# Kernel tuning notes

Hardware: AMD Instinct MI355X
Metric: run time of the kernel (lower is better)

Reference implementation:

```python
import jax, jax.numpy as jnp
import numpy as np

SEQ, BATCH, D_IN, D_HID, D_OUT = 2048, 256, 512, 512, 1000


def setup_inputs() -> dict:
    key = jax.random.key(0)
    ks = jax.random.split(key, 15)
    s_in = 1.0 / np.sqrt(D_IN)
    s_h = 1.0 / np.sqrt(D_HID)
    def lin(k, fan_in, shape, scale):
        return jax.random.uniform(k, shape, jnp.float32, -scale, scale)
    return {
        "x": jax.random.normal(ks[0], (SEQ, BATCH, D_IN), jnp.float32),
        # weights stored as [in, out] so y = x @ W + b
        "Wz": lin(ks[1], D_IN, (D_IN, D_HID), s_in),  "bz": lin(ks[2], D_IN, (D_HID,), s_in),
        "Uz": lin(ks[3], D_HID, (D_HID, D_HID), s_h), "buz": lin(ks[4], D_HID, (D_HID,), s_h),
        "Wr": lin(ks[5], D_IN, (D_IN, D_HID), s_in),  "br": lin(ks[6], D_IN, (D_HID,), s_in),
        "Ur": lin(ks[7], D_HID, (D_HID, D_HID), s_h), "bur": lin(ks[8], D_HID, (D_HID,), s_h),
        "Wh": lin(ks[9], D_IN, (D_IN, D_HID), s_in),  "bh": lin(ks[10], D_IN, (D_HID,), s_in),
        "Uh": lin(ks[11], D_HID, (D_HID, D_HID), s_h), "buh": lin(ks[12], D_HID, (D_HID,), s_h),
        "Wfc": lin(ks[13], D_HID, (D_HID, D_OUT), s_h), "bfc": lin(ks[14], D_HID, (D_OUT,), s_h),
    }


def reference(x, Wz, bz, Uz, buz, Wr, br, Ur, bur, Wh, bh, Uh, buh, Wfc, bfc):
    B, H = x.shape[1], Uz.shape[0]

    def gru_step(h, xt):
        # xt: [B, D_IN], h: [B, H]
        z = jax.nn.sigmoid(xt @ Wz + bz + h @ Uz + buz)
        r = jax.nn.sigmoid(xt @ Wr + br + h @ Ur + bur)
        h_tild = jnp.tanh(xt @ Wh + bh + (r * h) @ Uh + buh)
        h_new = (1.0 - z) * h + z * h_tild
        return h_new, None

    h0 = jnp.zeros((B, H), x.dtype)  # zero init hidden (broadcast-equivalent)
    h, _ = jax.lax.scan(gru_step, h0, x)
    out = jax.nn.relu(h) @ Wfc + bfc        # [B, D_OUT]
    out = out[None]                          # [1, B, D_OUT]
    return jax.nn.log_softmax(out, axis=1)  # dim=1 as in torch module
```

## Files before the change

kernel.cpp:

```cpp
#include <hip/hip_runtime.h>


typedef unsigned short ushort_t;
typedef unsigned int uint_t;
typedef __bf16 bf16_t;
typedef bf16_t bf16x8 __attribute__((ext_vector_type(8)));
typedef float f32x4 __attribute__((ext_vector_type(4)));
typedef uint_t u32x4 __attribute__((ext_vector_type(4)));

__device__ __forceinline__ ushort_t f2bf(float f) {
  uint_t u = __float_as_uint(f);
  u += 0x7FFFu + ((u >> 16) & 1u);
  return (ushort_t)(u >> 16);
}
__device__ __forceinline__ float bf2f(ushort_t h) {
  return __uint_as_float(((uint_t)h) << 16);
}

__device__ __forceinline__ uint_t atom_add_ret(uint_t* p, uint_t v) {
  uint_t old;
  asm volatile("global_atomic_add %0, %1, %2, off sc0\n\t"
               "s_waitcnt vmcnt(0)"
               : "=v"(old) : "v"(p), "v"(v) : "memory");
  return old;
}

__global__ __launch_bounds__(256) void prep_kernel(
    const float* __restrict__ Wz, const float* __restrict__ Wr, const float* __restrict__ Wh,
    const float* __restrict__ Uz, const float* __restrict__ Ur, const float* __restrict__ Uh,
    const float* __restrict__ bz, const float* __restrict__ buz,
    const float* __restrict__ br, const float* __restrict__ bur,
    const float* __restrict__ bh, const float* __restrict__ buh,
    ushort_t* __restrict__ UT, ushort_t* __restrict__ WT, float* __restrict__ gbias)
{
  const int idx = blockIdx.x * 256 + threadIdx.x;
  {
    const int gate = idx >> 18, n = (idx >> 9) & 511, k = idx & 511;
    const float* U = (gate == 0) ? Uz : (gate == 1 ? Ur : Uh);
    UT[idx] = f2bf(U[k * 512 + n]);
  }
  {
    const int n = idx >> 9, k = idx & 511;
    const int gate = n >> 9, nn = n & 511;
    const float* W = (gate == 0) ? Wz : (gate == 1 ? Wr : Wh);
    WT[idx] = f2bf(W[k * 512 + nn]);
  }
  if (idx < 1536) {
    const int gate = idx >> 9, nn = idx & 511;
    gbias[idx] = (gate == 0) ? (bz[nn] + buz[nn])
               : (gate == 1) ? (br[nn] + bur[nn])
                             : (bh[nn] + buh[nn]);
  }
}

__global__ __launch_bounds__(256) void gate_gemm(
    const float* __restrict__ x,
    const ushort_t* __restrict__ WT,
    const float* __restrict__ gbias,
    ushort_t* __restrict__ gout,
    int mtiles)
{
  __shared__ ushort_t A_sh[128 * 72];
  __shared__ ushort_t B_sh[128 * 72];
  const int bid = blockIdx.x;
  int mt, nt;
  if ((mtiles & 31) == 0) {
    const int sb = bid / 384;
    const int r = bid - sb * 384;
    mt = sb * 32 + (r & 31);
    nt = r >> 5;
  } else {
    mt = bid / 12;
    nt = bid - mt * 12;
  }
  const int mrow0 = mt * 128;
  const int ncol0 = nt * 128;
  const int tid = threadIdx.x;
  const int wid = tid >> 6;
  const int lane = tid & 63;
  const int wm = wid >> 1, wn = wid & 1;
  const int l15 = lane & 15, l4 = lane >> 4;

  const f32x4 vzero = {0.f, 0.f, 0.f, 0.f};
  f32x4 acc[4][4];
#pragma unroll
  for (int m = 0; m < 4; ++m) {
#pragma unroll
    for (int n = 0; n < 4; ++n) acc[m][n] = vzero;
  }

  const int ar = tid >> 4;
  const int ak = tid & 15;
  const int bn = tid >> 3;
  const int bk = tid & 7;

  for (int ks = 0; ks < 8; ++ks) {
    if (ks) __syncthreads();
    const int k0 = ks * 64;
#pragma unroll
    for (int p = 0; p < 8; ++p) {
      const int r = p * 16 + ar;
      const float4 v = *(const float4*)&x[(size_t)(mrow0 + r) * 512 + (k0 + ak * 4)];
      ushort4 hv;
      hv.x = f2bf(v.x); hv.y = f2bf(v.y); hv.z = f2bf(v.z); hv.w = f2bf(v.w);
      *(ushort4*)&A_sh[r * 72 + ak * 4] = hv;
    }
#pragma unroll
    for (int p = 0; p < 4; ++p) {
      const int n = p * 32 + bn;
      *(uint4*)&B_sh[n * 72 + bk * 8] =
          *(const uint4*)&WT[(size_t)(ncol0 + n) * 512 + (k0 + bk * 8)];
    }
    __syncthreads();
#pragma unroll
    for (int kk = 0; kk < 2; ++kk) {
      bf16x8 a[4], b[4];
#pragma unroll
      for (int m = 0; m < 4; ++m)
        a[m] = *(const bf16x8*)&A_sh[(wm * 64 + m * 16 + l15) * 72 + kk * 32 + l4 * 8];
#pragma unroll
      for (int n = 0; n < 4; ++n)
        b[n] = *(const bf16x8*)&B_sh[(wn * 64 + n * 16 + l15) * 72 + kk * 32 + l4 * 8];
#pragma unroll
      for (int m = 0; m < 4; ++m) {
#pragma unroll
        for (int n = 0; n < 4; ++n)
          acc[m][n] = __builtin_amdgcn_mfma_f32_16x16x32_bf16(a[m], b[n], acc[m][n], 0, 0, 0);
      }
    }
  }
#pragma unroll
  for (int n = 0; n < 4; ++n) {
    const int gcol = ncol0 + wn * 64 + n * 16 + l15;
    const float bv = gbias[gcol];
#pragma unroll
    for (int m = 0; m < 4; ++m) {
      const int grow = mrow0 + wm * 64 + m * 16 + l4 * 4;
#pragma unroll
      for (int q = 0; q < 4; ++q)
        gout[(size_t)(grow + q) * 1536 + gcol] = f2bf(acc[m][n][q] + bv);
    }
  }
}

__device__ __forceinline__ bool group_barrier(uint_t* ctr, uint_t target, int tid, int* s_dead) {
  asm volatile("s_waitcnt vmcnt(0)" ::: "memory");
  __syncthreads();
  if (tid == 0) {
    uint_t seen = atom_add_ret(ctr, 1u) + 1u;
    int cnt = 0;
    while (seen < target) {
      __builtin_amdgcn_s_sleep(1);
      seen = atom_add_ret(ctr, 0u);
      if (++cnt > (1 << 15)) { *s_dead = 1; break; }
    }
  }
  __syncthreads();
  return *s_dead != 0;
}

__device__ __forceinline__ void stage16x512(const ushort_t* __restrict__ src, int g,
                                            ushort_t* dst_lds, int tid) {
  const ushort_t* p[4];
#pragma unroll
  for (int k = 0; k < 4; ++k) {
    const int idx = tid + (k << 8);
    const int r = idx >> 6, kc = idx & 63;
    p[k] = src + (((g * 16 + r) << 9) + kc * 8);
  }
  u32x4 v0, v1, v2, v3;
  asm volatile(
      "global_load_dwordx4 %0, %4, off sc0\n\t"
      "global_load_dwordx4 %1, %5, off sc0\n\t"
      "global_load_dwordx4 %2, %6, off sc0\n\t"
      "global_load_dwordx4 %3, %7, off sc0\n\t"
      "s_waitcnt vmcnt(0)"
      : "=&v"(v0), "=&v"(v1), "=&v"(v2), "=&v"(v3)
      : "v"(p[0]), "v"(p[1]), "v"(p[2]), "v"(p[3])
      : "memory");
#pragma unroll
  for (int k = 0; k < 4; ++k) {
    const int idx = tid + (k << 8);
    const int r = idx >> 6, kc = idx & 63;
    *(u32x4*)&dst_lds[r * 520 + kc * 8] = (k == 0) ? v0 : (k == 1) ? v1 : (k == 2) ? v2 : v3;
  }
}

__global__ __launch_bounds__(256, 1) void gru_rec(
    const ushort_t* __restrict__ UT,
    const ushort_t* __restrict__ gates,
    ushort_t* __restrict__ h_buf,
    ushort_t* __restrict__ rh_buf,
    float* __restrict__ h_state,
    uint_t* __restrict__ bars,
    int Tc, int first)
{
  __shared__ ushort_t h_st[16 * 520];
  __shared__ float z_sh[512];
  __shared__ float hown[512];
  __shared__ float red[512];
  __shared__ int s_dead;

  const int tid = threadIdx.x;
  const int bid = blockIdx.x;
  const int g = bid & 15;
  const int j = bid >> 4;
  const int wid = tid >> 6;
  const int lane = tid & 63;
  const int l15 = lane & 15;
  const int l4 = lane >> 4;
  if (tid == 0) s_dead = 0;

  uint_t* ctr = bars + g * 64;
  uint_t nbar = 0;

  const int p1gate = wid >> 1;
  const int p1nt = wid & 1;
  const int p2nt = wid >> 1;
  const int p2kh = wid & 1;

  bf16x8 UB[16];
  {
    const size_t base = (size_t)((p1gate << 9) + j * 32 + p1nt * 16 + l15) * 512 + (size_t)(l4 * 8);
#pragma unroll
    for (int kk = 0; kk < 16; ++kk) UB[kk] = *(const bf16x8*)&UT[base + (size_t)kk * 32];
  }
  bf16x8 UH[8];
  {
    const size_t base = (size_t)(1024 + j * 32 + p2nt * 16 + l15) * 512 + (size_t)(p2kh * 256 + l4 * 8);
#pragma unroll
    for (int kk = 0; kk < 8; ++kk) UH[kk] = *(const bf16x8*)&UT[base + (size_t)kk * 32];
  }

  if (first) {
    for (int i = tid; i < 512; i += 256) {
      const int r = i >> 5, c = i & 31;
      h_buf[((g * 16 + r) << 9) + j * 32 + c] = 0;
      hown[i] = 0.f;
    }
  } else {
    for (int i = tid; i < 512; i += 256) {
      const int r = i >> 5, c = i & 31;
      hown[i] = h_state[((g * 16 + r) << 9) + j * 32 + c];
    }
  }
  if (group_barrier(ctr, (++nbar) * 16, tid, &s_dead)) return;

  const int colg1 = j * 32 + p1nt * 16 + l15;
  const int colg2 = j * 32 + p2nt * 16 + l15;

  float c1[4], c2[4], n1[4], n2[4];
  {
    const size_t gb = (size_t)(g * 16) * 1536;
#pragma unroll
    for (int q = 0; q < 4; ++q) {
      c1[q] = bf2f(gates[gb + (size_t)(l4 * 4 + q) * 1536 + (p1gate << 9) + colg1]);
      c2[q] = bf2f(gates[gb + (size_t)(l4 * 4 + q) * 1536 + 1024 + colg2]);
    }
  }

  for (int tt = 0; tt < Tc; ++tt) {
    stage16x512(h_buf, g, h_st, tid);
    __syncthreads();
    {
      const ushort_t* ap = &h_st[l15 * 520 + l4 * 8];
      f32x4 a0 = {0.f, 0.f, 0.f, 0.f}, a1 = {0.f, 0.f, 0.f, 0.f};
#pragma unroll
      for (int kk = 0; kk < 16; kk += 2) {
        a0 = __builtin_amdgcn_mfma_f32_16x16x32_bf16(*(const bf16x8*)(ap + kk * 32), UB[kk], a0, 0, 0, 0);
        a1 = __builtin_amdgcn_mfma_f32_16x16x32_bf16(*(const bf16x8*)(ap + kk * 32 + 32), UB[kk + 1], a1, 0, 0, 0);
      }
      const f32x4 acc = a0 + a1;
      const int lc = p1nt * 16 + l15;
#pragma unroll
      for (int q = 0; q < 4; ++q) {
        const int row = l4 * 4 + q;
        const float pre = acc[q] + c1[q];
        const float s = 1.f / (1.f + __expf(-pre));
        if (p1gate == 0) z_sh[row * 32 + lc] = s;
        else rh_buf[((g * 16 + row) << 9) + j * 32 + lc] = f2bf(s * hown[row * 32 + lc]);
      }
    }
    if (group_barrier(ctr, (++nbar) * 16, tid, &s_dead)) break;

    stage16x512(rh_buf, g, h_st, tid);
    __syncthreads();
    {
      const ushort_t* ap = &h_st[l15 * 520 + p2kh * 256 + l4 * 8];
      f32x4 a0 = {0.f, 0.f, 0.f, 0.f}, a1 = {0.f, 0.f, 0.f, 0.f};
#pragma unroll
      for (int kk = 0; kk < 8; kk += 2) {
        a0 = __builtin_amdgcn_mfma_f32_16x16x32_bf16(*(const bf16x8*)(ap + kk * 32), UH[kk], a0, 0, 0, 0);
        a1 = __builtin_amdgcn_mfma_f32_16x16x32_bf16(*(const bf16x8*)(ap + kk * 32 + 32), UH[kk + 1], a1, 0, 0, 0);
      }
      const f32x4 acc = a0 + a1;
      if (p2kh == 1) {
#pragma unroll
        for (int q = 0; q < 4; ++q) red[p2nt * 256 + (l4 * 4 + q) * 16 + l15] = acc[q];
      }
      if (tt + 1 < Tc) {
        const size_t gb = (size_t)((size_t)(tt + 1) * 256 + g * 16) * 1536;
#pragma unroll
        for (int q = 0; q < 4; ++q) {
          n1[q] = bf2f(gates[gb + (size_t)(l4 * 4 + q) * 1536 + (p1gate << 9) + colg1]);
          n2[q] = bf2f(gates[gb + (size_t)(l4 * 4 + q) * 1536 + 1024 + colg2]);
        }
      }
      __syncthreads();
      if (p2kh == 0) {
        const int lc = p2nt * 16 + l15;
#pragma unroll
        for (int q = 0; q < 4; ++q) {
          const int row = l4 * 4 + q;
          const float dot = acc[q] + red[p2nt * 256 + row * 16 + l15];
          float pre = dot + c2[q];
          pre = fminf(15.f, fmaxf(-15.f, pre));
          const float e = __expf(2.f * pre);
          const float th = (e - 1.f) / (e + 1.f);
          const float z = z_sh[row * 32 + lc];
          const float hold = hown[row * 32 + lc];
          const float hnew = (1.f - z) * hold + z * th;
          hown[row * 32 + lc] = hnew;
          h_buf[((g * 16 + row) << 9) + j * 32 + lc] = f2bf(hnew);
          if (tt == Tc - 1) h_state[((g * 16 + row) << 9) + j * 32 + lc] = hnew;
        }
      }
    }
    if (group_barrier(ctr, (++nbar) * 16, tid, &s_dead)) break;
#pragma unroll
    for (int q = 0; q < 4; ++q) { c1[q] = n1[q]; c2[q] = n2[q]; }
  }
}

__global__ __launch_bounds__(256) void fc_kernel(
    const float* __restrict__ h, const float* __restrict__ Wfc,
    const float* __restrict__ bfc, float* __restrict__ logits)
{
  __shared__ float hsh[16][520];
  const int tid = threadIdx.x;
  const int by = blockIdx.y;
  {
    const int r = tid >> 4, seg = tid & 15;
    const float* src = &h[(size_t)(by * 16 + r) * 512 + seg * 32];
#pragma unroll
    for (int i = 0; i < 8; ++i) {
      float4 v = *(const float4*)&src[i * 4];
      v.x = fmaxf(v.x, 0.f); v.y = fmaxf(v.y, 0.f);
      v.z = fmaxf(v.z, 0.f); v.w = fmaxf(v.w, 0.f);
      *(float4*)&hsh[r][seg * 32 + i * 4] = v;
    }
  }
  __syncthreads();
  const int c = tid & 63, rq = tid >> 6;
  const int gc = blockIdx.x * 64 + c;
  if (gc >= 1000) return;
  float acc0 = 0.f, acc1 = 0.f, acc2 = 0.f, acc3 = 0.f;
  for (int k = 0; k < 512; ++k) {
    const float w = Wfc[(size_t)k * 1000 + gc];
    acc0 += hsh[rq * 4 + 0][k] * w;
    acc1 += hsh[rq * 4 + 1][k] * w;
    acc2 += hsh[rq * 4 + 2][k] * w;
    acc3 += hsh[rq * 4 + 3][k] * w;
  }
  const float bv = bfc[gc];
  const int r0 = by * 16 + rq * 4;
  logits[(size_t)(r0 + 0) * 1000 + gc] = acc0 + bv;
  logits[(size_t)(r0 + 1) * 1000 + gc] = acc1 + bv;
  logits[(size_t)(r0 + 2) * 1000 + gc] = acc2 + bv;
  logits[(size_t)(r0 + 3) * 1000 + gc] = acc3 + bv;
}

__global__ __launch_bounds__(256) void lsm_kernel(const float* __restrict__ logits,
                                                  float* __restrict__ out)
{
  const int c = blockIdx.x, tid = threadIdx.x;
  const int wid = tid >> 6, lane = tid & 63;
  __shared__ float red[8];
  const float v = logits[(size_t)tid * 1000 + c];
  float m = v;
#pragma unroll
  for (int o = 32; o >= 1; o >>= 1) m = fmaxf(m, __shfl_xor(m, o));
  if (lane == 0) red[wid] = m;
  __syncthreads();
  m = fmaxf(fmaxf(red[0], red[1]), fmaxf(red[2], red[3]));
  float s = __expf(v - m);
#pragma unroll
  for (int o = 32; o >= 1; o >>= 1) s += __shfl_xor(s, o);
  if (lane == 0) red[4 + wid] = s;
  __syncthreads();
  s = red[4] + red[5] + red[6] + red[7];
  out[(size_t)tid * 1000 + c] = (v - m) - __logf(s);
}

extern "C" void kernel_launch(void* const* d_in, const int* in_sizes, int n_in,
                              void* d_out, int out_size, void* d_ws, size_t ws_size,
                              hipStream_t stream) {
  (void)in_sizes; (void)n_in; (void)out_size;
  const float* x   = (const float*)d_in[0];
  const float* Wz  = (const float*)d_in[1];
  const float* bz  = (const float*)d_in[2];
  const float* Uz  = (const float*)d_in[3];
  const float* buz = (const float*)d_in[4];
  const float* Wr  = (const float*)d_in[5];
  const float* br  = (const float*)d_in[6];
  const float* Ur  = (const float*)d_in[7];
  const float* bur = (const float*)d_in[8];
  const float* Wh  = (const float*)d_in[9];
  const float* bh  = (const float*)d_in[10];
  const float* Uh  = (const float*)d_in[11];
  const float* buh = (const float*)d_in[12];
  const float* Wfc = (const float*)d_in[13];
  const float* bfc = (const float*)d_in[14];
  float* out = (float*)d_out;
  char* ws = (char*)d_ws;

  ushort_t* UT     = (ushort_t*)(ws + 0);
  ushort_t* WT     = (ushort_t*)(ws + 1572864);
  float*    gbias  = (float*)(ws + 3145728);
  ushort_t* h_buf  = (ushort_t*)(ws + 3151872);
  ushort_t* rh_buf = (ushort_t*)(ws + 3414016);
  float*    hstate = (float*)(ws + 3676160);
  float*    logits = (float*)(ws + 4200448);
  uint_t*   bars   = (uint_t*)(ws + 5224448);
  ushort_t* gates  = (ushort_t*)(ws + 5228544);

  const size_t fixed = 5228544;
  const size_t per_step = (size_t)256 * 1536 * 2;
  int Tc_max = 2048;
  if (ws_size < fixed + (size_t)2048 * per_step) {
    const size_t avail = (ws_size > fixed) ? (ws_size - fixed) : 0;
    Tc_max = (int)(avail / per_step);
    Tc_max &= ~15;
    if (Tc_max < 16) Tc_max = 16;
  }

  prep_kernel<<<3072, 256, 0, stream>>>(Wz, Wr, Wh, Uz, Ur, Uh,
                                        bz, buz, br, bur, bh, buh, UT, WT, gbias);

  int done = 0;
  while (done < 2048) {
    const int Tc = (2048 - done < Tc_max) ? (2048 - done) : Tc_max;
    const int mtiles = Tc * 2;
    gate_gemm<<<mtiles * 12, 256, 0, stream>>>(x + (size_t)done * 256 * 512, WT, gbias, gates, mtiles);
    hipMemsetAsync(bars, 0, 4096, stream);
    gru_rec<<<256, 256, 0, stream>>>(UT, gates, h_buf, rh_buf, hstate, bars, Tc, done == 0 ? 1 : 0);
    done += Tc;
  }
  fc_kernel<<<dim3(16, 16), 256, 0, stream>>>(hstate, Wfc, bfc, logits);
  lsm_kernel<<<1000, 256, 0, stream>>>(logits, out);
}
```

Measured before the change: 10.73 ms.

## Overlap next-step gate prefetch with the cross-block barrier spin

Moves the prefetch of next-timestep precomputed gate inputs out of the second matmul phase and issues it as raw global_load_ushort instructions just before the final per-step group barrier, so the loads stay in flight while the block spins. The barrier arrival becomes a no-return atomic add followed by a separate polling loop. The aim is to hide gate-load latency behind synchronization and shorten the atomic round trip. It relies on inline asm with no waitcnt on the outstanding loads until the next barrier's vmcnt(0), and it duplicates the barrier logic inline.

```diff
diff --git a/kernel.cpp b/kernel.cpp
--- a/kernel.cpp
+++ b/kernel.cpp
@@ -13,8 +13,8 @@
   u += 0x7FFFu + ((u >> 16) & 1u);
   return (ushort_t)(u >> 16);
 }
-__device__ __forceinline__ float bf2f(ushort_t h) {
-  return __uint_as_float(((uint_t)h) << 16);
+__device__ __forceinline__ float bfu2f(uint_t h) {
+  return __uint_as_float(h << 16);
 }
 
 __device__ __forceinline__ uint_t atom_add_ret(uint_t* p, uint_t v) {
@@ -24,6 +24,12 @@
                : "=v"(old) : "v"(p), "v"(v) : "memory");
   return old;
 }
+__device__ __forceinline__ void atom_add_noret(uint_t* p, uint_t v) {
+  asm volatile("global_atomic_add %0, %1, off" :: "v"(p), "v"(v) : "memory");
+}
+
+#define GLOAD_U16(dst, ptr, off) \
+  asm volatile("global_load_ushort %0, %1, off offset:" #off : "=v"(dst) : "v"(ptr))
 
 __global__ __launch_bounds__(256) void prep_kernel(
     const float* __restrict__ Wz, const float* __restrict__ Wr, const float* __restrict__ Wh,
@@ -147,11 +153,12 @@
   asm volatile("s_waitcnt vmcnt(0)" ::: "memory");
   __syncthreads();
   if (tid == 0) {
-    uint_t seen = atom_add_ret(ctr, 1u) + 1u;
+    atom_add_noret(ctr, 1u);
     int cnt = 0;
-    while (seen < target) {
+    for (;;) {
+      const uint_t seen = atom_add_ret(ctr, 0u);
+      if (seen >= target) break;
       __builtin_amdgcn_s_sleep(1);
-      seen = atom_add_ret(ctr, 0u);
       if (++cnt > (1 << 15)) { *s_dead = 1; break; }
     }
   }
@@ -249,19 +256,21 @@
   const int colg1 = j * 32 + p1nt * 16 + l15;
   const int colg2 = j * 32 + p2nt * 16 + l15;
 
-  float c1[4], c2[4], n1[4], n2[4];
+  uint_t c1u[4], c2u[4], n1u[4], n2u[4];
   {
     const size_t gb = (size_t)(g * 16) * 1536;
 #pragma unroll
     for (int q = 0; q < 4; ++q) {
-      c1[q] = bf2f(gates[gb + (size_t)(l4 * 4 + q) * 1536 + (p1gate << 9) + colg1]);
-      c2[q] = bf2f(gates[gb + (size_t)(l4 * 4 + q) * 1536 + 1024 + colg2]);
+      n1u[q] = gates[gb + (size_t)(l4 * 4 + q) * 1536 + (p1gate << 9) + colg1];
+      n2u[q] = gates[gb + (size_t)(l4 * 4 + q) * 1536 + 1024 + colg2];
     }
   }
 
   for (int tt = 0; tt < Tc; ++tt) {
     stage16x512(h_buf, g, h_st, tid);
     __syncthreads();
+#pragma unroll
+    for (int q = 0; q < 4; ++q) { c1u[q] = n1u[q]; c2u[q] = n2u[q]; }
     {
       const ushort_t* ap = &h_st[l15 * 520 + l4 * 8];
       f32x4 a0 = {0.f, 0.f, 0.f, 0.f}, a1 = {0.f, 0.f, 0.f, 0.f};
@@ -275,7 +284,7 @@
 #pragma unroll
       for (int q = 0; q < 4; ++q) {
         const int row = l4 * 4 + q;
-        const float pre = acc[q] + c1[q];
+        const float pre = acc[q] + bfu2f(c1u[q]);
         const float s = 1.f / (1.f + __expf(-pre));
         if (p1gate == 0) z_sh[row * 32 + lc] = s;
         else rh_buf[((g * 16 + row) << 9) + j * 32 + lc] = f2bf(s * hown[row * 32 + lc]);
@@ -298,14 +307,6 @@
 #pragma unroll
         for (int q = 0; q < 4; ++q) red[p2nt * 256 + (l4 * 4 + q) * 16 + l15] = acc[q];
       }
-      if (tt + 1 < Tc) {
-        const size_t gb = (size_t)((size_t)(tt + 1) * 256 + g * 16) * 1536;
-#pragma unroll
-        for (int q = 0; q < 4; ++q) {
-          n1[q] = bf2f(gates[gb + (size_t)(l4 * 4 + q) * 1536 + (p1gate << 9) + colg1]);
-          n2[q] = bf2f(gates[gb + (size_t)(l4 * 4 + q) * 1536 + 1024 + colg2]);
-        }
-      }
       __syncthreads();
       if (p2kh == 0) {
         const int lc = p2nt * 16 + l15;
@@ -313,7 +314,7 @@
         for (int q = 0; q < 4; ++q) {
           const int row = l4 * 4 + q;
           const float dot = acc[q] + red[p2nt * 256 + row * 16 + l15];
-          float pre = dot + c2[q];
+          float pre = dot + bfu2f(c2u[q]);
           pre = fminf(15.f, fmaxf(-15.f, pre));
           const float e = __expf(2.f * pre);
           const float th = (e - 1.f) / (e + 1.f);
@@ -326,9 +327,35 @@
         }
       }
     }
-    if (group_barrier(ctr, (++nbar) * 16, tid, &s_dead)) break;
-#pragma unroll
-    for (int q = 0; q < 4; ++q) { c1[q] = n1[q]; c2[q] = n2[q]; }
+
+    asm volatile("s_waitcnt vmcnt(0)" ::: "memory");
+    if (tt + 1 < Tc) {
+      const size_t gb = (size_t)((size_t)(tt + 1) * 256 + g * 16) * 1536;
+      const ushort_t* b1  = &gates[gb + (size_t)(l4 * 4) * 1536 + (p1gate << 9) + colg1];
+      const ushort_t* b1c = b1 + 2 * 1536;
+      const ushort_t* b2  = &gates[gb + (size_t)(l4 * 4) * 1536 + 1024 + colg2];
+      const ushort_t* b2c = b2 + 2 * 1536;
+      GLOAD_U16(n1u[0], b1, 0);   GLOAD_U16(n1u[1], b1, 3072);
+      GLOAD_U16(n1u[2], b1c, 0);  GLOAD_U16(n1u[3], b1c, 3072);
+      GLOAD_U16(n2u[0], b2, 0);   GLOAD_U16(n2u[1], b2, 3072);
+      GLOAD_U16(n2u[2], b2c, 0);  GLOAD_U16(n2u[3], b2c, 3072);
+    }
+    __syncthreads();
+    if (tid == 0) {
+      atom_add_noret(ctr, 1u);
+      const uint_t target = (++nbar) * 16;
+      int cnt = 0;
+      for (;;) {
+        const uint_t seen = atom_add_ret(ctr, 0u);
+        if (seen >= target) break;
+        __builtin_amdgcn_s_sleep(1);
+        if (++cnt > (1 << 15)) { s_dead = 1; break; }
+      }
+    } else {
+      ++nbar;
+    }
+    __syncthreads();
+    if (s_dead) break;
   }
 }
 
```

New measurement: 9.957 ms. -7.2%, faster.
